# Optimization experiments

Hardware: AMD Instinct MI355X
Metric: run time of the kernel (lower is better)

Reference implementation:

```python
import jax, jax.numpy as jnp
import numpy as np

H = 512      # hidden_size / feature_dim (hard-coded in Net)
H2 = 256     # hidden // 2 in encoder stem
V = 32000    # vocab_size = out_shape[0]
EPS = 1e-5   # BatchNorm eps (torch default)


def _conv(x, w, stride, pad, groups=1):
    return jax.lax.conv_general_dilated(
        x, w, (stride, stride), ((pad, pad), (pad, pad)),
        feature_group_count=groups,
        dimension_numbers=('NCHW', 'OIHW', 'NCHW'))


def _bn(x, g, b):
    # training-mode BatchNorm: biased batch statistics over (N,H,W)
    m = jnp.mean(x, axis=(0, 2, 3), keepdims=True)
    v = jnp.mean((x - m) ** 2, axis=(0, 2, 3), keepdims=True)
    return (x - m) * jax.lax.rsqrt(v + EPS) * g[None, :, None, None] + b[None, :, None, None]


def _encoder(images, conv1_w, bn1_g, bn1_b, dw_w, pw_w, bn2_g, bn2_b,
             se_fc1_w, se_fc2_w, enc_fc_w, enc_fc_b):
    x = jax.nn.relu(_bn(_conv(images, conv1_w, 2, 1), bn1_g, bn1_b))   # [B,256,112,112]
    x = _conv(x, dw_w, 1, 1, groups=H2)                                 # depthwise 3x3
    x = _conv(x, pw_w, 1, 0)                                            # pointwise -> [B,512,112,112]
    x = jax.nn.relu(_bn(x, bn2_g, bn2_b))
    y = jnp.mean(x, axis=(2, 3))                                        # SE squeeze [B,512]
    y = jax.nn.relu(y @ se_fc1_w.T) @ se_fc2_w.T
    x = x * jax.nn.sigmoid(y)[:, :, None, None]                         # SE excite
    f = jnp.mean(x, axis=(2, 3))                                        # AdaptiveAvgPool2d(1)
    return f @ enc_fc_w.T + enc_fc_b                                    # [B,512]


def _decode(feats, inputs, embed, q_w, k_w, v_w,
            gru_w_ih, gru_w_hh, gru_b_ih, gru_b_hh, fc_w, fc_b):
    B = feats.shape[0]
    # Attention over a single feature 'key' (r=1): softmax over one element
    # is exactly 1, so ctx = v(feats), independent of h and of t. q_w/k_w
    # therefore do not influence the output (their gradients are exactly 0).
    ctx = feats @ v_w.T                                                 # [B,512]
    embs = jnp.take(embed, inputs, axis=0)                              # [B,T,512]
    h0 = jnp.zeros((B, H), feats.dtype)

    def step(h, emb_t):
        x = jnp.concatenate([emb_t, ctx], axis=-1)                      # [B,1024]
        gi = x @ gru_w_ih.T + gru_b_ih                                  # [B,1536]
        gh = h @ gru_w_hh.T + gru_b_hh
        ir, iz, inn = jnp.split(gi, 3, axis=-1)
        hr, hz, hn = jnp.split(gh, 3, axis=-1)
        r = jax.nn.sigmoid(ir + hr)
        z = jax.nn.sigmoid(iz + hz)
        n = jnp.tanh(inn + r * hn)
        h_new = (1.0 - z) * n + z * h                                   # torch GRUCell update
        return h_new, h_new @ fc_w.T + fc_b                             # per-step logits [B,V]

    _, logits = jax.lax.scan(step, h0, jnp.swapaxes(embs, 0, 1))        # [T,B,V]
    return jnp.swapaxes(logits, 0, 1)                                   # [B,T,V]


def setup_inputs() -> dict:
    key = jax.random.key(0)
    ks = jax.random.split(key, 16)
    s = 0.02
    B, Tc = 16, 33
    return {
        'images': jax.random.normal(ks[0], (B, 3, 224, 224), jnp.float32),
        'captions': jax.random.randint(ks[1], (B, Tc), 0, V),
        'conv1_w': jax.random.normal(ks[2], (H2, 3, 3, 3), jnp.float32) * s,
        'bn1_g': jnp.ones((H2,), jnp.float32),
        'bn1_b': jnp.zeros((H2,), jnp.float32),
        'dw_w': jax.random.normal(ks[3], (H2, 1, 3, 3), jnp.float32) * s,
        'pw_w': jax.random.normal(ks[4], (H, H2, 1, 1), jnp.float32) * s,
        'bn2_g': jnp.ones((H,), jnp.float32),
        'bn2_b': jnp.zeros((H,), jnp.float32),
        'se_fc1_w': jax.random.normal(ks[5], (H // 4, H), jnp.float32) * s,
        'se_fc2_w': jax.random.normal(ks[6], (H, H // 4), jnp.float32) * s,
        'enc_fc_w': jax.random.normal(ks[7], (H, H), jnp.float32) * s,
        'enc_fc_b': jnp.zeros((H,), jnp.float32),
        'embed': jax.random.normal(ks[8], (V, H), jnp.float32) * s,
        'q_w': jax.random.normal(ks[9], (H, H), jnp.float32) * s,
        'k_w': jax.random.normal(ks[10], (H, H), jnp.float32) * s,
        'v_w': jax.random.normal(ks[11], (H, H), jnp.float32) * s,
        'gru_w_ih': jax.random.normal(ks[12], (3 * H, 2 * H), jnp.float32) * s,
        'gru_w_hh': jax.random.normal(ks[13], (3 * H, H), jnp.float32) * s,
        'gru_b_ih': jnp.zeros((3 * H,), jnp.float32),
        'gru_b_hh': jnp.zeros((3 * H,), jnp.float32),
        'fc_w': jax.random.normal(ks[14], (V, H), jnp.float32) * s,
        'fc_b': jnp.zeros((V,), jnp.float32),
    }


def reference(images, captions, conv1_w, bn1_g, bn1_b, dw_w, pw_w, bn2_g, bn2_b,
              se_fc1_w, se_fc2_w, enc_fc_w, enc_fc_b, embed, q_w, k_w, v_w,
              gru_w_ih, gru_w_hh, gru_b_ih, gru_b_hh, fc_w, fc_b):
    feats = _encoder(images, conv1_w, bn1_g, bn1_b, dw_w, pw_w, bn2_g, bn2_b,
                     se_fc1_w, se_fc2_w, enc_fc_w, enc_fc_b)
    inputs = captions[:, :-1]                                           # teacher forcing
    return _decode(feats, inputs, embed, q_w, k_w, v_w,
                   gru_w_ih, gru_w_hh, gru_b_ih, gru_b_hh, fc_w, fc_b)
```

## Files before the change

kernel.cpp:

```cpp
#include <hip/hip_runtime.h>

typedef unsigned int u32;
typedef unsigned short u16;
typedef unsigned long long u64;
typedef short bf16x8 __attribute__((ext_vector_type(8)));
typedef float f32x4 __attribute__((ext_vector_type(4)));

#define S1 12544
#define NSTAT 200704
#define EPS 1e-5f
#define AP 264

__device__ __forceinline__ u16 f2bf(float f) {
  union { float f; u32 u; } x; x.f = f;
  u32 r = x.u + 0x7fffu + ((x.u >> 16) & 1u);
  return (u16)(r >> 16);
}
__device__ __forceinline__ void bf2x2(u32 u, float& lo, float& hi) {
  union { u32 u; float f; } a, b;
  a.u = u << 16; b.u = u & 0xffff0000u;
  lo = a.f; hi = b.f;
}
__device__ __forceinline__ float sigm(float x) { return 1.f / (1.f + expf(-x)); }

#define CW 225
__global__ __launch_bounds__(256) void k_conv1(const float* __restrict__ img,
    const float* __restrict__ w, u16* __restrict__ out, float* __restrict__ stats) {
  int blk = blockIdx.x;
  int b = blk / 56, strip = blk - b * 56;
  int r0 = strip * 2;
  int c = threadIdx.x;
  __shared__ float simg[3 * 5 * CW];
  const float* ib = img + (size_t)b * 3 * 224 * 224;
  for (int i = c; i < 3 * 5 * CW; i += 256) {
    int ch = i / (5 * CW);
    int rem = i - ch * (5 * CW);
    int lr = rem / CW;
    int col = rem - lr * CW;
    int ih = 2 * r0 - 1 + lr;
    int iw = col - 1;
    float v = 0.f;
    if (ih >= 0 && ih < 224 && iw >= 0 && iw < 224) v = ib[((size_t)ch * 224 + ih) * 224 + iw];
    simg[i] = v;
  }
  float wr[27];
#pragma unroll
  for (int i = 0; i < 27; i++) wr[i] = w[c * 27 + i];
  __syncthreads();
  float s = 0.f, q = 0.f;
  for (int orow = 0; orow < 2; orow++) {
    int oh = r0 + orow;
    for (int ow = 0; ow < 112; ow++) {
      float acc = 0.f;
#pragma unroll
      for (int ch = 0; ch < 3; ch++)
#pragma unroll
        for (int dr = 0; dr < 3; dr++) {
          const float* rp = &simg[(ch * 5 + 2 * orow + dr) * CW + 2 * ow];
          acc = fmaf(wr[(ch * 3 + dr) * 3 + 0], rp[0], acc);
          acc = fmaf(wr[(ch * 3 + dr) * 3 + 1], rp[1], acc);
          acc = fmaf(wr[(ch * 3 + dr) * 3 + 2], rp[2], acc);
        }
      s += acc; q = fmaf(acc, acc, q);
      out[((size_t)(b * 112 + oh) * 112 + ow) * 256 + c] = f2bf(acc);
    }
  }
  atomicAdd(&stats[c], s);
  atomicAdd(&stats[256 + c], q);
}

__global__ void k_bnfin(const float* __restrict__ stats, const float* __restrict__ g,
                        const float* __restrict__ bb, float* __restrict__ par, int C, float invN) {
  int c = blockIdx.x * 256 + threadIdx.x;
  if (c < C) {
    float m = stats[c] * invN;
    float v = stats[C + c] * invN - m * m;
    float sc = g[c] * rsqrtf(v + EPS);
    par[c] = sc;
    par[C + c] = bb[c] - m * sc;
  }
}

__global__ void k_cvt4(const float* __restrict__ w, u16* __restrict__ o, int n4) {
  int i = blockIdx.x * 256 + threadIdx.x;
  if (i < n4) {
    float4 v = ((const float4*)w)[i];
    union { u16 h[4]; uint2 u; } pk;
    pk.h[0] = f2bf(v.x); pk.h[1] = f2bf(v.y); pk.h[2] = f2bf(v.z); pk.h[3] = f2bf(v.w);
    ((uint2*)o)[i] = pk.u;
  }
}

#define LD_COL(ohv, iwv, slot) do {                                          \
    int _oh = (ohv), _iw = (iwv);                                            \
  _Pragma("unroll")                                                          \
    for (int _dr = 0; _dr < 3; _dr++) {                                      \
      int _ih = _oh - 1 + _dr;                                               \
      float _x0 = 0.f, _x1 = 0.f, _x2 = 0.f, _x3 = 0.f;                      \
      if (_ih >= 0 && _ih < 112 && _iw >= 0 && _iw < 112) {                  \
        uint2 _v = *(const uint2*)(ib + ((size_t)(_ih * 112 + _iw)) * 256 + c4); \
        float _t0, _t1, _t2, _t3;                                            \
        bf2x2(_v.x, _t0, _t1); bf2x2(_v.y, _t2, _t3);                        \
        _x0 = fmaxf(fmaf(_t0, sc[0], sh[0]), 0.f);                           \
        _x1 = fmaxf(fmaf(_t1, sc[1], sh[1]), 0.f);                           \
        _x2 = fmaxf(fmaf(_t2, sc[2], sh[2]), 0.f);                           \
        _x3 = fmaxf(fmaf(_t3, sc[3], sh[3]), 0.f);                           \
      }                                                                      \
      act[_dr][slot][0] = _x0; act[_dr][slot][1] = _x1;                      \
      act[_dr][slot][2] = _x2; act[_dr][slot][3] = _x3;                      \
    }                                                                        \
  } while (0)

__global__ __launch_bounds__(256) void k_dws(const u16* __restrict__ cin,
    const float* __restrict__ bn1p, const float* __restrict__ dww, u16* __restrict__ out) {
  int tid = threadIdx.x;
  int wave = tid >> 6, lane = tid & 63;
  int c4 = lane * 4;
  int m0 = blockIdx.x * 64;
  int bimg = blockIdx.x / 196;
  float sc[4], sh[4], w9[4][9];
#pragma unroll
  for (int cc = 0; cc < 4; cc++) {
    sc[cc] = bn1p[c4 + cc];
    sh[cc] = bn1p[256 + c4 + cc];
#pragma unroll
    for (int i = 0; i < 9; i++) w9[cc][i] = dww[(c4 + cc) * 9 + i];
  }
  const u16* ib = cin + (size_t)bimg * S1 * 256;
  float act[3][3][4];
#pragma unroll
  for (int pp = 0; pp < 16; pp++) {
    int p = wave * 16 + pp;
    int s = m0 + p - bimg * S1;
    int oh = s / 112, ow = s - oh * 112;
    if (pp == 0 || ow == 0) {
      LD_COL(oh, ow - 1, (pp + 0) % 3);
      LD_COL(oh, ow,     (pp + 1) % 3);
      LD_COL(oh, ow + 1, (pp + 2) % 3);
    } else {
      LD_COL(oh, ow + 1, (pp + 2) % 3);
    }
    float a0 = 0.f, a1 = 0.f, a2 = 0.f, a3 = 0.f;
#pragma unroll
    for (int dr = 0; dr < 3; dr++)
#pragma unroll
      for (int dc = 0; dc < 3; dc++) {
        const int sl = (pp + dc) % 3;
        const int wi = dr * 3 + dc;
        a0 = fmaf(w9[0][wi], act[dr][sl][0], a0);
        a1 = fmaf(w9[1][wi], act[dr][sl][1], a1);
        a2 = fmaf(w9[2][wi], act[dr][sl][2], a2);
        a3 = fmaf(w9[3][wi], act[dr][sl][3], a3);
      }
    union { u16 h[4]; uint2 v; } pk;
    pk.h[0] = f2bf(a0); pk.h[1] = f2bf(a1);
    pk.h[2] = f2bf(a2); pk.h[3] = f2bf(a3);
    *(uint2*)(out + (size_t)(m0 + p) * 256 + c4) = pk.v;
  }
}

__global__ __launch_bounds__(256, 2) void k_pws(const u16* __restrict__ A,
    const u16* __restrict__ bwb, float* __restrict__ partials,
    const float* __restrict__ bn2p, int pass) {
  __shared__ u16 ash[64 * 256];
  int tid = threadIdx.x;
  int wave = tid >> 6, lane = tid & 63;
  int m0 = blockIdx.x * 64;
  {
    const char* gb = (const char*)(A + (size_t)m0 * 256);
    char* lb = (char*)ash;
#pragma unroll
    for (int i = 0; i < 8; i++) {
      int L = wave * 8192 + i * 1024 + lane * 16;
      int p = L >> 9;
      int gp = (L >> 4) & 31;
      int g = gp ^ (p & 7);
      uint4 v = *(const uint4*)(gb + (size_t)p * 512 + g * 16);
      *(uint4*)(lb + L) = v;
    }
  }
  __syncthreads();

  int quad = lane >> 4;
  int lr = lane & 15;
  int nbase = wave * 128;
  const char* ashb = (const char*)ash;
  f32x4 acc[4][8];
#pragma unroll
  for (int mt = 0; mt < 4; mt++)
#pragma unroll
    for (int nt = 0; nt < 8; nt++) acc[mt][nt] = (f32x4){0.f, 0.f, 0.f, 0.f};

#pragma unroll
  for (int ch = 0; ch < 8; ch++) {
    bf16x8 af[4];
#pragma unroll
    for (int mt = 0; mt < 4; mt++) {
      int row = mt * 16 + lr;
      int g = (ch * 4 + quad) ^ (row & 7);
      af[mt] = *(const bf16x8*)(ashb + row * 512 + g * 16);
    }
    bf16x8 bfr[8];
#pragma unroll
    for (int nt = 0; nt < 8; nt++)
      bfr[nt] = *(const bf16x8*)(bwb + (size_t)(nbase + nt * 16 + lr) * 256 + ch * 32 + quad * 8);
#pragma unroll
    for (int mt = 0; mt < 4; mt++)
#pragma unroll
      for (int nt = 0; nt < 8; nt++)
        acc[mt][nt] = __builtin_amdgcn_mfma_f32_16x16x32_bf16(af[mt], bfr[nt], acc[mt][nt], 0, 0, 0);
  }

  if (pass == 0) {
#pragma unroll
    for (int nt = 0; nt < 8; nt++) {
      float s = 0.f, q = 0.f;
#pragma unroll
      for (int mt = 0; mt < 4; mt++)
#pragma unroll
        for (int r = 0; r < 4; r++) {
          float v = acc[mt][nt][r];
          s += v; q = fmaf(v, v, q);
        }
      s += __shfl_xor(s, 16); s += __shfl_xor(s, 32);
      q += __shfl_xor(q, 16); q += __shfl_xor(q, 32);
      if (lane < 16) {
        int n = nbase + nt * 16 + lane;
        partials[(size_t)blockIdx.x * 1024 + n] = s;
        partials[(size_t)blockIdx.x * 1024 + 512 + n] = q;
      }
    }
  } else {
#pragma unroll
    for (int nt = 0; nt < 8; nt++) {
      int n = nbase + nt * 16 + lr;
      float scn = bn2p[n], shn = bn2p[512 + n];
      float s = 0.f;
#pragma unroll
      for (int mt = 0; mt < 4; mt++)
#pragma unroll
        for (int r = 0; r < 4; r++)
          s += fmaxf(fmaf(acc[mt][nt][r], scn, shn), 0.f);
      s += __shfl_xor(s, 16); s += __shfl_xor(s, 32);
      if (lane < 16)
        partials[(size_t)blockIdx.x * 512 + n] = s;
    }
  }
}

__global__ __launch_bounds__(256, 2) void k_pwpass(
    const u16* __restrict__ conv1out, const float* __restrict__ bn1p,
    const float* __restrict__ dww, const u16* __restrict__ bwb,
    float* __restrict__ partials, const float* __restrict__ bn2p, int pass) {
  __shared__ u16 ash[64 * AP];
  int tid = threadIdx.x;
  int wave = tid >> 6;
  int lane = tid & 63;
  int m0 = blockIdx.x * 64;
  int bimg = blockIdx.x / 196;
  {
    int c4 = lane * 4;
    float sc[4], sh[4], w9[4][9];
#pragma unroll
    for (int cc = 0; cc < 4; cc++) {
      sc[cc] = bn1p[c4 + cc];
      sh[cc] = bn1p[256 + c4 + cc];
#pragma unroll
      for (int i = 0; i < 9; i++) w9[cc][i] = dww[(c4 + cc) * 9 + i];
    }
    const u16* ib = conv1out + (size_t)bimg * S1 * 256;
    float act[3][3][4];
#pragma unroll
    for (int pp = 0; pp < 16; pp++) {
      int p = wave * 16 + pp;
      int s = m0 + p - bimg * S1;
      int oh = s / 112, ow = s - oh * 112;
      if (pp == 0 || ow == 0) {
        LD_COL(oh, ow - 1, (pp + 0) % 3);
        LD_COL(oh, ow,     (pp + 1) % 3);
        LD_COL(oh, ow + 1, (pp + 2) % 3);
      } else {
        LD_COL(oh, ow + 1, (pp + 2) % 3);
      }
      float a0 = 0.f, a1 = 0.f, a2 = 0.f, a3 = 0.f;
#pragma unroll
      for (int dr = 0; dr < 3; dr++)
#pragma unroll
        for (int dc = 0; dc < 3; dc++) {
          const int sl = (pp + dc) % 3;
          const int wi = dr * 3 + dc;
          a0 = fmaf(w9[0][wi], act[dr][sl][0], a0);
          a1 = fmaf(w9[1][wi], act[dr][sl][1], a1);
          a2 = fmaf(w9[2][wi], act[dr][sl][2], a2);
          a3 = fmaf(w9[3][wi], act[dr][sl][3], a3);
        }
      union { u16 h[4]; uint2 v; } pk;
      pk.h[0] = f2bf(a0); pk.h[1] = f2bf(a1);
      pk.h[2] = f2bf(a2); pk.h[3] = f2bf(a3);
      *(uint2*)(&ash[p * AP + c4]) = pk.v;
    }
  }
  __syncthreads();
  int quad = lane >> 4;
  int lr = lane & 15;
  int nbase = wave * 128;
  f32x4 acc[4][8];
#pragma unroll
  for (int mt = 0; mt < 4; mt++)
#pragma unroll
    for (int nt = 0; nt < 8; nt++) acc[mt][nt] = (f32x4){0.f, 0.f, 0.f, 0.f};
  for (int kk = 0; kk < 256; kk += 32) {
    bf16x8 af[4];
#pragma unroll
    for (int mt = 0; mt < 4; mt++)
      af[mt] = *(const bf16x8*)(&ash[(mt * 16 + lr) * AP + kk + quad * 8]);
    bf16x8 bfr[8];
#pragma unroll
    for (int nt = 0; nt < 8; nt++)
      bfr[nt] = *(const bf16x8*)(bwb + (size_t)(nbase + nt * 16 + lr) * 256 + kk + quad * 8);
#pragma unroll
    for (int mt = 0; mt < 4; mt++)
#pragma unroll
      for (int nt = 0; nt < 8; nt++)
        acc[mt][nt] = __builtin_amdgcn_mfma_f32_16x16x32_bf16(af[mt], bfr[nt], acc[mt][nt], 0, 0, 0);
  }
  if (pass == 0) {
#pragma unroll
    for (int nt = 0; nt < 8; nt++) {
      float s = 0.f, q = 0.f;
#pragma unroll
      for (int mt = 0; mt < 4; mt++)
#pragma unroll
        for (int r = 0; r < 4; r++) {
          float v = acc[mt][nt][r];
          s += v; q = fmaf(v, v, q);
        }
      s += __shfl_xor(s, 16); s += __shfl_xor(s, 32);
      q += __shfl_xor(q, 16); q += __shfl_xor(q, 32);
      if (lane < 16) {
        int n = nbase + nt * 16 + lane;
        partials[(size_t)blockIdx.x * 1024 + n] = s;
        partials[(size_t)blockIdx.x * 1024 + 512 + n] = q;
      }
    }
  } else {
#pragma unroll
    for (int nt = 0; nt < 8; nt++) {
      int n = nbase + nt * 16 + lr;
      float scn = bn2p[n], shn = bn2p[512 + n];
      float s = 0.f;
#pragma unroll
      for (int mt = 0; mt < 4; mt++)
#pragma unroll
        for (int r = 0; r < 4; r++)
          s += fmaxf(fmaf(acc[mt][nt][r], scn, shn), 0.f);
      s += __shfl_xor(s, 16); s += __shfl_xor(s, 32);
      if (lane < 16)
        partials[(size_t)blockIdx.x * 512 + n] = s;
    }
  }
}

__global__ __launch_bounds__(256) void k_red1(const float* __restrict__ P, float* __restrict__ P2) {
  int blk = blockIdx.x;
  int t = threadIdx.x;
  float4 s = {0.f, 0.f, 0.f, 0.f};
  for (int r = 0; r < 49; r++) {
    float4 v = *(const float4*)(P + ((size_t)(blk * 49 + r)) * 1024 + t * 4);
    s.x += v.x; s.y += v.y; s.z += v.z; s.w += v.w;
  }
  *(float4*)(P2 + (size_t)blk * 1024 + t * 4) = s;
}

__global__ void k_red_bn2(const float* __restrict__ P2, const float* __restrict__ g,
                          const float* __restrict__ bb, float* __restrict__ par) {
  int c = blockIdx.x * 256 + threadIdx.x;
  float s = 0.f, q = 0.f;
  for (int i = 0; i < 64; i++) {
    s += P2[(size_t)i * 1024 + c];
    q += P2[(size_t)i * 1024 + 512 + c];
  }
  float m = s * (1.f / (float)NSTAT);
  float v = q * (1.f / (float)NSTAT) - m * m;
  float sc = g[c] * rsqrtf(v + EPS);
  par[c] = sc;
  par[512 + c] = bb[c] - m * sc;
}

__global__ void k_red_y(const float* __restrict__ P, float* __restrict__ yb) {
  int idx = blockIdx.x * 256 + threadIdx.x;
  int b = idx >> 9, c = idx & 511;
  float s = 0.f;
  for (int i = 0; i < 196; i++) s += P[(size_t)(b * 196 + i) * 512 + c];
  yb[idx] = s;
}

__global__ __launch_bounds__(256) void k_se(const float* __restrict__ y,
    const float* __restrict__ se1, const float* __restrict__ se2,
    const float* __restrict__ encw, const float* __restrict__ encb,
    const float* __restrict__ vw, float* __restrict__ ctxb) {
  int b = blockIdx.x;
  int t = threadIdx.x;
  __shared__ __align__(16) float ybar[512];
  __shared__ __align__(16) float uu[128];
  __shared__ __align__(16) float ff[512];
  __shared__ __align__(16) float feats[512];
  for (int i = t; i < 512; i += 256) ybar[i] = y[b * 512 + i] * (1.f / 12544.f);
  __syncthreads();
  if (t < 128) {
    const float4* wr = (const float4*)(se1 + t * 512);
    const float4* xv = (const float4*)ybar;
    float a = 0.f;
    for (int k = 0; k < 128; k++) {
      float4 w4 = wr[k], x4 = xv[k];
      a = fmaf(w4.x, x4.x, a); a = fmaf(w4.y, x4.y, a);
      a = fmaf(w4.z, x4.z, a); a = fmaf(w4.w, x4.w, a);
    }
    uu[t] = fmaxf(a, 0.f);
  }
  __syncthreads();
  for (int c = t; c < 512; c += 256) {
    const float4* wr = (const float4*)(se2 + c * 128);
    const float4* xv = (const float4*)uu;
    float a = 0.f;
    for (int k = 0; k < 32; k++) {
      float4 w4 = wr[k], x4 = xv[k];
      a = fmaf(w4.x, x4.x, a); a = fmaf(w4.y, x4.y, a);
      a = fmaf(w4.z, x4.z, a); a = fmaf(w4.w, x4.w, a);
    }
    ff[c] = ybar[c] * sigm(a);
  }
  __syncthreads();
  for (int c = t; c < 512; c += 256) {
    const float4* wr = (const float4*)(encw + (size_t)c * 512);
    const float4* xv = (const float4*)ff;
    float a = encb[c];
    for (int k = 0; k < 128; k++) {
      float4 w4 = wr[k], x4 = xv[k];
      a = fmaf(w4.x, x4.x, a); a = fmaf(w4.y, x4.y, a);
      a = fmaf(w4.z, x4.z, a); a = fmaf(w4.w, x4.w, a);
    }
    feats[c] = a;
  }
  __syncthreads();
  for (int c = t; c < 512; c += 256) {
    const float4* wr = (const float4*)(vw + (size_t)c * 512);
    const float4* xv = (const float4*)feats;
    float a = 0.f;
    for (int k = 0; k < 128; k++) {
      float4 w4 = wr[k], x4 = xv[k];
      a = fmaf(w4.x, x4.x, a); a = fmaf(w4.y, x4.y, a);
      a = fmaf(w4.z, x4.z, a); a = fmaf(w4.w, x4.w, a);
    }
    ctxb[b * 512 + c] = a;
  }
}

__global__ __launch_bounds__(256) void k_gctx(const float* __restrict__ ctxb,
    const float* __restrict__ wih, const float* __restrict__ bih, float* __restrict__ gictx) {
  int lb = threadIdx.x >> 4;
  int lj = threadIdx.x & 15;
  int j = blockIdx.x * 16 + lj;
  const float4* wr = (const float4*)(wih + (size_t)j * 1024 + 512);
  const float4* xv = (const float4*)(ctxb + lb * 512);
  float a = bih[j];
#pragma unroll 4
  for (int k = 0; k < 128; k++) {
    float4 w4 = wr[k], x4 = xv[k];
    a = fmaf(w4.x, x4.x, a); a = fmaf(w4.y, x4.y, a);
    a = fmaf(w4.z, x4.z, a); a = fmaf(w4.w, x4.w, a);
  }
  gictx[lb * 1536 + j] = a;
}

__global__ __launch_bounds__(256) void k_gi2(const int* __restrict__ caps,
    const float* __restrict__ embed, const float* __restrict__ wih,
    const float* __restrict__ gictx, float* __restrict__ gi) {
  int tt = blockIdx.x;
  int jt = blockIdx.y;
  int lb = threadIdx.x >> 4;
  int lj = threadIdx.x & 15;
  int j = jt * 16 + lj;
  int tok = caps[lb * 33 + tt];
  const float4* wr = (const float4*)(wih + (size_t)j * 1024);
  const float4* xv = (const float4*)(embed + (size_t)tok * 512);
  float a = gictx[lb * 1536 + j];
#pragma unroll 4
  for (int k = 0; k < 128; k++) {
    float4 w4 = wr[k], x4 = xv[k];
    a = fmaf(w4.x, x4.x, a); a = fmaf(w4.y, x4.y, a);
    a = fmaf(w4.z, x4.z, a); a = fmaf(w4.w, x4.w, a);
  }
  gi[((size_t)tt * 16 + lb) * 1536 + j] = a;
}

__global__ __launch_bounds__(192) void k_gru_step(const float* __restrict__ whh,
    const float* __restrict__ bhh, const float* __restrict__ gi_t,
    const float* __restrict__ h_in, float* __restrict__ h_out) {
  int g = blockIdx.x;
  int tid = threadIdx.x;
  int s = tid / 24;
  int r = tid - s * 24;
  int gate = r >> 3, lj = r & 7;
  int jj = g * 8 + lj;
  int R = gate * 512 + jj;
  float4 w[16];
  {
    const float4* wp = (const float4*)(whh + (size_t)R * 512 + s * 64);
#pragma unroll
    for (int i = 0; i < 16; i++) w[i] = wp[i];
  }
  __shared__ __align__(16) float hs[16][512];
  __shared__ float pr[8][24][16];

  {
    const float4* hp = (const float4*)h_in;
    float4* hd = (float4*)&hs[0][0];
    for (int i = tid; i < 2048; i += 192) hd[i] = hp[i];
  }
  __syncthreads();
#pragma unroll
  for (int b = 0; b < 16; b++) {
    const float4* hv = (const float4*)&hs[b][s * 64];
    float a = 0.f;
#pragma unroll
    for (int k = 0; k < 16; k++) {
      float4 w4 = w[k], h4 = hv[k];
      a = fmaf(w4.x, h4.x, a); a = fmaf(w4.y, h4.y, a);
      a = fmaf(w4.z, h4.z, a); a = fmaf(w4.w, h4.w, a);
    }
    pr[s][r][b] = a;
  }
  __syncthreads();
  if (tid < 128) {
    int b = tid >> 3, jl = tid & 7;
    int j = g * 8 + jl;
    float gh[3];
#pragma unroll
    for (int gg = 0; gg < 3; gg++) {
      int rr = gg * 8 + jl;
      float sum = bhh[gg * 512 + j];
#pragma unroll
      for (int ss = 0; ss < 8; ss++) sum += pr[ss][rr][b];
      gh[gg] = sum;
    }
    const float* gib = gi_t + (size_t)b * 1536;
    float rg = sigm(gib[j] + gh[0]);
    float z  = sigm(gib[j + 512] + gh[1]);
    float n  = tanhf(gib[j + 1024] + rg * gh[2]);
    float hp = hs[b][j];
    h_out[b * 512 + j] = (1.f - z) * n + z * hp;
  }
}

__global__ __launch_bounds__(256) void k_fc(const float* __restrict__ A,
    const u16* __restrict__ Bwb, const float* __restrict__ bias, float* __restrict__ out) {
  __shared__ u16 ash[128 * 136];
  int tid = threadIdx.x;
  int wave = tid >> 6;
  int lane = tid & 63;
  int quad = lane >> 4;
  int lr = lane & 15;
  int N0 = blockIdx.x * 256;
  int M0 = blockIdx.y * 128;
  f32x4 acc[8][4];
#pragma unroll
  for (int mf = 0; mf < 8; mf++)
#pragma unroll
    for (int nf = 0; nf < 4; nf++) acc[mf][nf] = (f32x4){0.f, 0.f, 0.f, 0.f};
  int arow = tid >> 1;
  int acol = (tid & 1) * 64;
  for (int kc = 0; kc < 512; kc += 128) {
#pragma unroll
    for (int j = 0; j < 16; j++) {
      float4 v = *(const float4*)(A + (size_t)(M0 + arow) * 512 + kc + acol + j * 4);
      union { u16 h[4]; uint2 u; } pk;
      pk.h[0] = f2bf(v.x); pk.h[1] = f2bf(v.y); pk.h[2] = f2bf(v.z); pk.h[3] = f2bf(v.w);
      *(uint2*)(&ash[arow * 136 + acol + j * 4]) = pk.u;
    }
    __syncthreads();
#pragma unroll
    for (int ks = 0; ks < 128; ks += 32) {
      bf16x8 af[8];
#pragma unroll
      for (int mf = 0; mf < 8; mf++)
        af[mf] = *(const bf16x8*)(&ash[(mf * 16 + lr) * 136 + ks + quad * 8]);
      bf16x8 bf[4];
#pragma unroll
      for (int nf = 0; nf < 4; nf++) {
        int n = N0 + wave * 64 + nf * 16 + lr;
        bf[nf] = *(const bf16x8*)(Bwb + (size_t)n * 512 + kc + ks + quad * 8);
      }
#pragma unroll
      for (int mf = 0; mf < 8; mf++)
#pragma unroll
        for (int nf = 0; nf < 4; nf++)
          acc[mf][nf] = __builtin_amdgcn_mfma_f32_16x16x32_bf16(af[mf], bf[nf], acc[mf][nf], 0, 0, 0);
    }
    __syncthreads();
  }
#pragma unroll
  for (int nf = 0; nf < 4; nf++) {
    int j = N0 + wave * 64 + nf * 16 + lr;
    float bv = bias[j];
#pragma unroll
    for (int mf = 0; mf < 8; mf++)
#pragma unroll
      for (int r = 0; r < 4; r++) {
        int m = M0 + mf * 16 + quad * 4 + r;
        int orow = (m & 15) * 32 + (m >> 4);
        out[(size_t)orow * 32000 + j] = acc[mf][nf][r] + bv;
      }
  }
}

extern "C" void kernel_launch(void* const* d_in, const int* in_sizes, int n_in,
                              void* d_out, int out_size, void* d_ws, size_t ws_size,
                              hipStream_t stream) {
  const float* images  = (const float*)d_in[0];
  const int*   caps    = (const int*)d_in[1];
  const float* conv1_w = (const float*)d_in[2];
  const float* bn1_g   = (const float*)d_in[3];
  const float* bn1_b   = (const float*)d_in[4];
  const float* dw_w    = (const float*)d_in[5];
  const float* pw_w    = (const float*)d_in[6];
  const float* bn2_g   = (const float*)d_in[7];
  const float* bn2_b   = (const float*)d_in[8];
  const float* se1     = (const float*)d_in[9];
  const float* se2     = (const float*)d_in[10];
  const float* encw    = (const float*)d_in[11];
  const float* encb    = (const float*)d_in[12];
  const float* embed   = (const float*)d_in[13];
  const float* vw      = (const float*)d_in[16];
  const float* wih     = (const float*)d_in[17];
  const float* whh     = (const float*)d_in[18];
  const float* bih     = (const float*)d_in[19];
  const float* bhh     = (const float*)d_in[20];
  const float* fcw     = (const float*)d_in[21];
  const float* fcb     = (const float*)d_in[22];
  float* out = (float*)d_out;

  const bool big = ws_size >= (size_t)230 * 1000 * 1000;

  char* ws = (char*)d_ws;
  size_t off = 0;
  auto alloc = [&](size_t bytes) {
    void* p = ws + off;
    off = (off + bytes + 255) & ~(size_t)255;
    return p;
  };
  u16* conv1out = (u16*)alloc((size_t)51380224 * 2);
  u16* fcwb     = (u16*)conv1out;
  u16* dwout    = big ? (u16*)alloc((size_t)51380224 * 2) : (u16*)nullptr;
  u16* bwb      = (u16*)alloc((size_t)131072 * 2);
  float* partials = (float*)alloc((size_t)3136 * 1024 * 4);
  float* p2     = (float*)alloc((size_t)64 * 1024 * 4);
  float* stats1 = (float*)alloc(512 * 4);
  float* h_all  = (float*)alloc((size_t)33 * 8192 * 4);
  float* bn1p   = (float*)alloc(512 * 4);
  float* bn2p   = (float*)alloc(1024 * 4);
  float* yb     = (float*)alloc(8192 * 4);
  float* ctxb   = (float*)alloc(8192 * 4);
  float* gictx  = (float*)alloc((size_t)16 * 1536 * 4);
  float* gi     = (float*)alloc((size_t)32 * 16 * 1536 * 4);
  (void)in_sizes; (void)n_in; (void)out_size;

  hipMemsetAsync(stats1, 0, 512 * 4, stream);
  hipMemsetAsync(h_all, 0, 8192 * 4, stream);

  k_conv1<<<896, 256, 0, stream>>>(images, conv1_w, conv1out, stats1);
  k_bnfin<<<1, 256, 0, stream>>>(stats1, bn1_g, bn1_b, bn1p, 256, 1.f / (float)NSTAT);
  k_cvt4<<<128, 256, 0, stream>>>(pw_w, bwb, 32768);

  if (big) {
    k_dws<<<3136, 256, 0, stream>>>(conv1out, bn1p, dw_w, dwout);
    k_cvt4<<<16000, 256, 0, stream>>>(fcw, fcwb, 4096000);
    k_pws<<<3136, 256, 0, stream>>>(dwout, bwb, partials, bn2p, 0);
    k_red1<<<64, 256, 0, stream>>>(partials, p2);
    k_red_bn2<<<2, 256, 0, stream>>>(p2, bn2_g, bn2_b, bn2p);
    k_pws<<<3136, 256, 0, stream>>>(dwout, bwb, partials, bn2p, 1);
  } else {
    k_pwpass<<<3136, 256, 0, stream>>>(conv1out, bn1p, dw_w, bwb, partials, bn2p, 0);
    k_red1<<<64, 256, 0, stream>>>(partials, p2);
    k_red_bn2<<<2, 256, 0, stream>>>(p2, bn2_g, bn2_b, bn2p);
    k_pwpass<<<3136, 256, 0, stream>>>(conv1out, bn1p, dw_w, bwb, partials, bn2p, 1);
    k_cvt4<<<16000, 256, 0, stream>>>(fcw, fcwb, 4096000);
  }
  k_red_y<<<32, 256, 0, stream>>>(partials, yb);
  k_se<<<16, 256, 0, stream>>>(yb, se1, se2, encw, encb, vw, ctxb);
  k_gctx<<<96, 256, 0, stream>>>(ctxb, wih, bih, gictx);
  dim3 ggi(32, 96);
  k_gi2<<<ggi, 256, 0, stream>>>(caps, embed, wih, gictx, gi);
  for (int t = 0; t < 32; t++)
    k_gru_step<<<64, 192, 0, stream>>>(whh, bhh, gi + (size_t)t * 16 * 1536,
                                       h_all + (size_t)t * 8192, h_all + (size_t)(t + 1) * 8192);
  dim3 gfc(125, 4);
  k_fc<<<gfc, 256, 0, stream>>>(h_all + 8192, fcwb, fcb, out);
}
```

Measured before the change: 1.386 ms.

## Restructure embedding input-gate GEMV to wave-per-row with register-held weights

```diff
diff --git a/kernel.cpp b/kernel.cpp
--- a/kernel.cpp
+++ b/kernel.cpp
@@ -473,25 +473,30 @@
   gictx[lb * 1536 + j] = a;
 }
 
-__global__ __launch_bounds__(256) void k_gi2(const int* __restrict__ caps,
+__global__ __launch_bounds__(256) void k_gi3(const int* __restrict__ caps,
     const float* __restrict__ embed, const float* __restrict__ wih,
     const float* __restrict__ gictx, float* __restrict__ gi) {
-  int tt = blockIdx.x;
-  int jt = blockIdx.y;
-  int lb = threadIdx.x >> 4;
-  int lj = threadIdx.x & 15;
-  int j = jt * 16 + lj;
-  int tok = caps[lb * 33 + tt];
-  const float4* wr = (const float4*)(wih + (size_t)j * 1024);
-  const float4* xv = (const float4*)(embed + (size_t)tok * 512);
-  float a = gictx[lb * 1536 + j];
-#pragma unroll 4
-  for (int k = 0; k < 128; k++) {
-    float4 w4 = wr[k], x4 = xv[k];
-    a = fmaf(w4.x, x4.x, a); a = fmaf(w4.y, x4.y, a);
-    a = fmaf(w4.z, x4.z, a); a = fmaf(w4.w, x4.w, a);
-  }
-  gi[((size_t)tt * 16 + lb) * 1536 + j] = a;
+  int wave = threadIdx.x >> 6, lane = threadIdx.x & 63;
+  int j = blockIdx.x * 4 + wave;
+  int t0 = blockIdx.y * 8;
+  const float4* wr = (const float4*)(wih + (size_t)j * 1024 + lane * 8);
+  float4 w0 = wr[0], w1 = wr[1];
+  for (int tt = t0; tt < t0 + 8; tt++) {
+#pragma unroll 2
+    for (int b = 0; b < 16; b++) {
+      int tok = caps[b * 33 + tt];
+      const float4* xv = (const float4*)(embed + (size_t)tok * 512 + lane * 8);
+      float4 x0 = xv[0], x1 = xv[1];
+      float a = w0.x * x0.x;
+      a = fmaf(w0.y, x0.y, a); a = fmaf(w0.z, x0.z, a); a = fmaf(w0.w, x0.w, a);
+      a = fmaf(w1.x, x1.x, a); a = fmaf(w1.y, x1.y, a);
+      a = fmaf(w1.z, x1.z, a); a = fmaf(w1.w, x1.w, a);
+#pragma unroll
+      for (int m = 1; m < 64; m <<= 1) a += __shfl_xor(a, m);
+      if (lane == 0)
+        gi[((size_t)tt * 16 + b) * 1536 + j] = a + gictx[b * 1536 + j];
+    }
+  }
 }
 
 __global__ __launch_bounds__(192) void k_gru_step(const float* __restrict__ whh,
@@ -689,8 +694,8 @@
   k_red_y<<<32, 256, 0, stream>>>(partials, yb);
   k_se<<<16, 256, 0, stream>>>(yb, se1, se2, encw, encb, vw, ctxb);
   k_gctx<<<96, 256, 0, stream>>>(ctxb, wih, bih, gictx);
-  dim3 ggi(32, 96);
-  k_gi2<<<ggi, 256, 0, stream>>>(caps, embed, wih, gictx, gi);
+  dim3 ggi3(384, 4);
+  k_gi3<<<ggi3, 256, 0, stream>>>(caps, embed, wih, gictx, gi);
   for (int t = 0; t < 32; t++)
     k_gru_step<<<64, 192, 0, stream>>>(whh, bhh, gi + (size_t)t * 16 * 1536,
                                        h_all + (size_t)t * 8192, h_all + (size_t)(t + 1) * 8192);
```

Measured after the change: 1.288 ms. 7.1% less time.
